# Performance work log

Hardware: AMD Instinct MI355X
Metric: run time of the kernel (lower is better)

Reference implementation:

```python
import jax, jax.numpy as jnp
import numpy as np

DIM = 1024
HEADS = 16
DIM_HEAD = 64
INNER = HEADS * DIM_HEAD
B, N = 2, 2048


def setup_inputs() -> dict:
    key = jax.random.key(0)
    ks = jax.random.split(key, 5)
    x = jax.random.normal(ks[0], (B, N, DIM), dtype=jnp.float32)
    ln_gamma = jnp.ones((DIM,), dtype=jnp.float32)
    ln_beta = jnp.zeros((DIM,), dtype=jnp.float32)
    # torch Linear: weight [out, in]; store as [in, out] for x @ W
    W_qkv = jax.random.normal(ks[1], (DIM, 3 * INNER), dtype=jnp.float32) * (DIM ** -0.5)
    W_out = jax.random.normal(ks[2], (INNER, DIM), dtype=jnp.float32) * (INNER ** -0.5)
    b_out = jax.random.normal(ks[3], (DIM,), dtype=jnp.float32) * 0.01
    return {"x": x, "ln_gamma": ln_gamma, "ln_beta": ln_beta,
            "W_qkv": W_qkv, "W_out": W_out, "b_out": b_out}


def reference(x, ln_gamma, ln_beta, W_qkv, W_out, b_out):
    eps = 1e-5
    scale = DIM_HEAD ** -0.5
    # LayerNorm over last dim
    mu = jnp.mean(x, axis=-1, keepdims=True)
    var = jnp.mean((x - mu) ** 2, axis=-1, keepdims=True)
    xn = (x - mu) * jax.lax.rsqrt(var + eps) * ln_gamma + ln_beta
    # QKV projection (no bias), split
    qkv = xn @ W_qkv                               # [B, N, 3*inner]
    q, k, v = jnp.split(qkv, 3, axis=-1)           # each [B, N, inner]
    def heads(t):
        return t.reshape(B, N, HEADS, DIM_HEAD).transpose(0, 2, 1, 3)  # [B, H, N, d]
    q, k, v = heads(q), heads(k), heads(v)
    dots = jnp.einsum("bhnd,bhmd->bhnm", q, k) * scale
    a = jax.nn.softmax(dots, axis=-1)
    out = jnp.einsum("bhnm,bhmd->bhnd", a, v)      # [B, H, N, d]
    out = out.transpose(0, 2, 1, 3).reshape(B, N, INNER)
    return out @ W_out + b_out                     # dropout p=0 -> identity
```

## Files before the change

kernel.cpp:

```cpp
#include <hip/hip_runtime.h>

typedef unsigned short U16;
typedef __bf16 bf16x8 __attribute__((ext_vector_type(8)));
typedef float f32x4 __attribute__((ext_vector_type(4)));

__device__ inline float b2f(U16 u) {
    union { unsigned int i; float f; } v;
    v.i = ((unsigned int)u) << 16;
    return v.f;
}
__device__ inline U16 f2b(float f) {
    union { float f; unsigned int u; } v;
    v.f = f;
    unsigned int r = (v.u + 0x7fffu + ((v.u >> 16) & 1u)) >> 16;
    return (U16)r;
}

__device__ inline void gld16(const void* g, void* l) {
    __builtin_amdgcn_global_load_lds(
        (const __attribute__((address_space(1))) void*)g,
        (__attribute__((address_space(3))) void*)l, 16, 0, 0);
}

__global__ void transpose_f2b(const float* __restrict__ in, U16* __restrict__ out,
                              int R, int C) {
    __shared__ float tile[32][33];
    int c0 = blockIdx.x * 32, r0 = blockIdx.y * 32;
    int tx = threadIdx.x, ty = threadIdx.y;
#pragma unroll
    for (int i = 0; i < 32; i += 8)
        tile[ty + i][tx] = in[(size_t)(r0 + ty + i) * C + c0 + tx];
    __syncthreads();
#pragma unroll
    for (int i = 0; i < 32; i += 8)
        out[(size_t)(c0 + ty + i) * R + r0 + tx] = f2b(tile[tx][ty + i]);
}

__global__ __launch_bounds__(256) void ln_kernel(const float* __restrict__ x,
                                                 const float* __restrict__ gamma,
                                                 const float* __restrict__ beta,
                                                 U16* __restrict__ xn) {
    int row = blockIdx.x;
    int t = threadIdx.x;
    float4 raw = ((const float4*)(x + (size_t)row * 1024))[t];
    float v[4] = { raw.x, raw.y, raw.z, raw.w };
    float s = v[0] + v[1] + v[2] + v[3];
    float s2 = v[0] * v[0] + v[1] * v[1] + v[2] * v[2] + v[3] * v[3];
#pragma unroll
    for (int off = 32; off >= 1; off >>= 1) {
        s  += __shfl_xor(s,  off);
        s2 += __shfl_xor(s2, off);
    }
    __shared__ float red[8];
    if ((t & 63) == 0) { red[(t >> 6) * 2] = s; red[(t >> 6) * 2 + 1] = s2; }
    __syncthreads();
    float S  = red[0] + red[2] + red[4] + red[6];
    float S2 = red[1] + red[3] + red[5] + red[7];
    float mu = S * (1.0f / 1024.0f);
    float var = S2 * (1.0f / 1024.0f) - mu * mu;
    float rstd = rsqrtf(var + 1e-5f);
    float4 g4 = ((const float4*)gamma)[t];
    float4 b4 = ((const float4*)beta)[t];
    ushort4 o;
    o.x = f2b((v[0] - mu) * rstd * g4.x + b4.x);
    o.y = f2b((v[1] - mu) * rstd * g4.y + b4.y);
    o.z = f2b((v[2] - mu) * rstd * g4.z + b4.z);
    o.w = f2b((v[3] - mu) * rstd * g4.w + b4.w);
    ((ushort4*)(xn + (size_t)row * 1024))[t] = o;
}

template <typename OutT>
__global__ __launch_bounds__(256) void gemm_bt(const U16* __restrict__ A,
                                               const U16* __restrict__ Bt,
                                               const float* __restrict__ bias,
                                               OutT* __restrict__ C,
                                               U16* __restrict__ vT,
                                               int M, int N, int K) {
    __shared__ __align__(16) U16 As[128 * 32];
    __shared__ __align__(16) U16 Bs[128 * 32];
    const int m0 = blockIdx.y * 128, n0 = blockIdx.x * 128;
    const int t = threadIdx.x;
    const int wave = t >> 6, lane = t & 63, l15 = lane & 15, quad = lane >> 4;
    const int wm = (wave >> 1) * 64, wn = (wave & 1) * 64;

    f32x4 acc[4][4];
#pragma unroll
    for (int i = 0; i < 4; i++)
#pragma unroll
        for (int j = 0; j < 4; j++)
            acc[i][j] = (f32x4){0.f, 0.f, 0.f, 0.f};

    const int c0i = t, c1i = 256 + t;
    const int r0 = c0i >> 2, kq0 = c0i & 3;
    const int r1 = c1i >> 2, kq1 = c1i & 3;

    for (int k0 = 0; k0 < K; k0 += 32) {
        gld16(&A[(size_t)(m0 + r0) * K + k0 + kq0 * 8], &As[c0i * 8]);
        gld16(&Bt[(size_t)(n0 + r0) * K + k0 + kq0 * 8], &Bs[c0i * 8]);
        gld16(&A[(size_t)(m0 + r1) * K + k0 + kq1 * 8], &As[c1i * 8]);
        gld16(&Bt[(size_t)(n0 + r1) * K + k0 + kq1 * 8], &Bs[c1i * 8]);
        __syncthreads();
        bf16x8 af[4], bfr[4];
#pragma unroll
        for (int i = 0; i < 4; i++)
            af[i] = *(const bf16x8*)&As[(wm + i * 16 + l15) * 32 + quad * 8];
#pragma unroll
        for (int j = 0; j < 4; j++)
            bfr[j] = *(const bf16x8*)&Bs[(wn + j * 16 + l15) * 32 + quad * 8];
#pragma unroll
        for (int i = 0; i < 4; i++)
#pragma unroll
            for (int j = 0; j < 4; j++)
                acc[i][j] = __builtin_amdgcn_mfma_f32_16x16x32_bf16(
                    af[i], bfr[j], acc[i][j], 0, 0, 0);
        __syncthreads();
    }
    if (vT && n0 >= 2048) {
#pragma unroll
        for (int i = 0; i < 4; i++) {
#pragma unroll
            for (int j = 0; j < 4; j++) {
                int col = n0 + wn + j * 16 + l15 - 2048;
                int hh = col >> 6, dd = col & 63;
                int row0 = m0 + wm + i * 16 + quad * 4;
                int bb = row0 >> 11, nn = row0 & 2047;
                ushort4 st;
                st.x = f2b(acc[i][j][0]); st.y = f2b(acc[i][j][1]);
                st.z = f2b(acc[i][j][2]); st.w = f2b(acc[i][j][3]);
                *(ushort4*)&vT[((((size_t)bb * 16) + hh) * 64 + dd) * 2048 + nn] = st;
            }
        }
        return;
    }
#pragma unroll
    for (int i = 0; i < 4; i++) {
#pragma unroll
        for (int j = 0; j < 4; j++) {
            int col = n0 + wn + j * 16 + l15;
            float bv = bias ? bias[col] : 0.0f;
#pragma unroll
            for (int r = 0; r < 4; r++) {
                int row = m0 + wm + i * 16 + quad * 4 + r;
                float val = acc[i][j][r] + bv;
                if constexpr (sizeof(OutT) == 4)
                    C[(size_t)row * N + col] = val;
                else
                    C[(size_t)row * N + col] = f2b(val);
            }
        }
    }
}

#define PSTR 72
__global__ __launch_bounds__(256) void attn_kernel(const U16* __restrict__ qkv,
                                                   const U16* __restrict__ vT,
                                                   U16* __restrict__ attn_out) {
    const int qt = blockIdx.x;
    const int bh = blockIdx.y;
    const int b = bh >> 4, h = bh & 15;
    const int t = threadIdx.x;
    const int wave = t >> 6, lane = t & 63, l15 = lane & 15, quad = lane >> 4;
    const float sc2 = 0.125f * 1.44269504089f;

    __shared__ __align__(16) U16 Kt[2][64 * 64];
    __shared__ __align__(16) U16 Vt[2][64 * 64];
    __shared__ __align__(16) U16 Pb[4][32 * PSTR];

    const size_t base = (size_t)(b * 2048) * 3072;
    const U16* vTbh = vT + ((size_t)(b * 16 + h) * 64) * 2048;

    bf16x8 qf[2][2];
#pragma unroll
    for (int rf = 0; rf < 2; rf++) {
        int qrow = qt * 128 + wave * 32 + rf * 16 + l15;
        const U16* qp = qkv + base + (size_t)qrow * 3072 + h * 64;
        qf[rf][0] = *(const bf16x8*)&qp[quad * 8];
        qf[rf][1] = *(const bf16x8*)&qp[32 + quad * 8];
    }

    float l_i[2][4];
    f32x4 o[2][4];
#pragma unroll
    for (int rf = 0; rf < 2; rf++) {
#pragma unroll
        for (int r = 0; r < 4; r++) l_i[rf][r] = 0.0f;
#pragma unroll
        for (int f = 0; f < 4; f++) o[rf][f] = (f32x4){0.f, 0.f, 0.f, 0.f};
    }

    const int c0 = t, c1 = 256 + t;
    const int row0 = c0 >> 3, oct0 = (c0 & 7) ^ (row0 & 7);
    const int row1 = c1 >> 3, oct1 = (c1 & 7) ^ (row1 & 7);
    const int s0 = (quad ^ (l15 & 7)) * 8;

    gld16(&qkv[base + (size_t)row0 * 3072 + 1024 + h * 64 + oct0 * 8], &Kt[0][c0 * 8]);
    gld16(&qkv[base + (size_t)row1 * 3072 + 1024 + h * 64 + oct1 * 8], &Kt[0][c1 * 8]);
    gld16(&vTbh[(size_t)row0 * 2048 + oct0 * 8], &Vt[0][c0 * 8]);
    gld16(&vTbh[(size_t)row1 * 2048 + oct1 * 8], &Vt[0][c1 * 8]);
    __syncthreads();

    for (int kt = 0; kt < 32; kt++) {
        {
            int nt = (kt + 1) & 31, nb = (kt + 1) & 1;
            gld16(&qkv[base + (size_t)(nt * 64 + row0) * 3072 + 1024 + h * 64 + oct0 * 8], &Kt[nb][c0 * 8]);
            gld16(&qkv[base + (size_t)(nt * 64 + row1) * 3072 + 1024 + h * 64 + oct1 * 8], &Kt[nb][c1 * 8]);
            gld16(&vTbh[(size_t)row0 * 2048 + nt * 64 + oct0 * 8], &Vt[nb][c0 * 8]);
            gld16(&vTbh[(size_t)row1 * 2048 + nt * 64 + oct1 * 8], &Vt[nb][c1 * 8]);
        }
        const U16* KtC = &Kt[kt & 1][0];
        const U16* VtC = &Vt[kt & 1][0];

        bf16x8 k0[4], k1[4];
#pragma unroll
        for (int c = 0; c < 4; c++) {
            k0[c] = *(const bf16x8*)&KtC[(c * 16 + l15) * 64 + s0];
            k1[c] = *(const bf16x8*)&KtC[(c * 16 + l15) * 64 + (s0 ^ 32)];
        }
        U16* pb = &Pb[wave][0];
#pragma unroll
        for (int rf = 0; rf < 2; rf++) {
            f32x4 s[4];
#pragma unroll
            for (int c = 0; c < 4; c++) {
                f32x4 z = (f32x4){0.f, 0.f, 0.f, 0.f};
                z = __builtin_amdgcn_mfma_f32_16x16x32_bf16(qf[rf][0], k0[c], z, 0, 0, 0);
                z = __builtin_amdgcn_mfma_f32_16x16x32_bf16(qf[rf][1], k1[c], z, 0, 0, 0);
                s[c] = z;
            }
#pragma unroll
            for (int r = 0; r < 4; r++) {
#pragma unroll
                for (int c = 0; c < 4; c++) {
                    float p = __builtin_amdgcn_exp2f(s[c][r] * sc2);
                    l_i[rf][r] += p;
                    union { float f; unsigned int u; } cv; cv.f = p;
                    pb[(rf * 16 + quad * 4 + r) * PSTR + c * 16 + l15] = (U16)(cv.u >> 16);
                }
            }
        }

        asm volatile("s_waitcnt lgkmcnt(0)" ::: "memory");

        bf16x8 vf0[4], vf1[4];
#pragma unroll
        for (int f = 0; f < 4; f++) {
            vf0[f] = *(const bf16x8*)&VtC[(f * 16 + l15) * 64 + s0];
            vf1[f] = *(const bf16x8*)&VtC[(f * 16 + l15) * 64 + (s0 ^ 32)];
        }
#pragma unroll
        for (int rf = 0; rf < 2; rf++) {
            bf16x8 pf0 = *(const bf16x8*)&pb[(rf * 16 + l15) * PSTR + quad * 8];
            bf16x8 pf1 = *(const bf16x8*)&pb[(rf * 16 + l15) * PSTR + 32 + quad * 8];
#pragma unroll
            for (int f = 0; f < 4; f++) {
                o[rf][f] = __builtin_amdgcn_mfma_f32_16x16x32_bf16(pf0, vf0[f], o[rf][f], 0, 0, 0);
                o[rf][f] = __builtin_amdgcn_mfma_f32_16x16x32_bf16(pf1, vf1[f], o[rf][f], 0, 0, 0);
            }
        }
        __syncthreads();
    }

#pragma unroll
    for (int rf = 0; rf < 2; rf++) {
#pragma unroll
        for (int r = 0; r < 4; r++) {
            float l = l_i[rf][r];
#pragma unroll
            for (int off = 8; off >= 1; off >>= 1)
                l += __shfl_xor(l, off, 16);
            l_i[rf][r] = 1.0f / l;
        }
#pragma unroll
        for (int f = 0; f < 4; f++) {
#pragma unroll
            for (int r = 0; r < 4; r++) {
                int row = b * 2048 + qt * 128 + wave * 32 + rf * 16 + quad * 4 + r;
                int col = h * 64 + f * 16 + l15;
                attn_out[(size_t)row * 1024 + col] = f2b(o[rf][f][r] * l_i[rf][r]);
            }
        }
    }
}

extern "C" void kernel_launch(void* const* d_in, const int* in_sizes, int n_in,
                              void* d_out, int out_size, void* d_ws, size_t ws_size,
                              hipStream_t stream) {
    (void)in_sizes; (void)n_in; (void)out_size; (void)ws_size;
    const float* x    = (const float*)d_in[0];
    const float* g    = (const float*)d_in[1];
    const float* be   = (const float*)d_in[2];
    const float* Wqkv = (const float*)d_in[3];
    const float* Wout = (const float*)d_in[4];
    const float* bout = (const float*)d_in[5];
    float* out = (float*)d_out;
    char* ws = (char*)d_ws;

    U16* xn   = (U16*)(ws);
    U16* qkv  = (U16*)(ws + (size_t)(8u  << 20));
    U16* WqT  = (U16*)(ws + (size_t)(32u << 20));
    U16* WoT  = (U16*)(ws + (size_t)(38u << 20));
    U16* vT   = (U16*)(ws + (size_t)(40u << 20));
    U16* aout = xn;

    transpose_f2b<<<dim3(3072 / 32, 1024 / 32), dim3(32, 8), 0, stream>>>(Wqkv, WqT, 1024, 3072);
    transpose_f2b<<<dim3(1024 / 32, 1024 / 32), dim3(32, 8), 0, stream>>>(Wout, WoT, 1024, 1024);
    ln_kernel<<<4096, 256, 0, stream>>>(x, g, be, xn);
    gemm_bt<U16><<<dim3(3072 / 128, 4096 / 128), 256, 0, stream>>>(xn, WqT, nullptr, qkv, vT, 4096, 3072, 1024);
    attn_kernel<<<dim3(16, 32), 256, 0, stream>>>(qkv, vT, aout);
    gemm_bt<float><<<dim3(1024 / 128, 4096 / 128), 256, 0, stream>>>(aout, WoT, bout, out, nullptr, 4096, 1024, 1024);
}
```

Before: 217.3 us.

## Split attention over KV halves with merge kernel, XCD-aware block mapping and setprio

Splits each attention block's 32 KV tiles into two halves processed by separate blocks, doubling the grid to 1024 blocks. Each half writes unnormalized fp32 partial outputs and row sums, and a new merge kernel adds them, normalizes, and writes bf16. This is valid without max-subtraction because the softmax uses no running max, so the partials combine by simple addition. It also remaps block IDs so the heads are grouped per XCD for L2 locality, hoists the V fragment loads earlier, and wraps the MFMA sections in s_setprio. The cost is extra fp32 global traffic, since partials go through the output buffer and workspace, plus one more kernel launch.

```diff
diff --git a/kernel.cpp b/kernel.cpp
--- a/kernel.cpp
+++ b/kernel.cpp
@@ -154,9 +154,16 @@
 #define PSTR 72
 __global__ __launch_bounds__(256) void attn_kernel(const U16* __restrict__ qkv,
                                                    const U16* __restrict__ vT,
-                                                   U16* __restrict__ attn_out) {
-    const int qt = blockIdx.x;
-    const int bh = blockIdx.y;
+                                                   float* __restrict__ po0,
+                                                   float* __restrict__ po1,
+                                                   float* __restrict__ pl) {
+    const int p = blockIdx.x;
+    const int xcd = p & 7;
+    const int slot = p >> 3;
+    const int bh = ((slot & 3) << 3) | xcd;
+    const int r2 = slot >> 2;
+    const int qt = r2 & 15;
+    const int half = r2 >> 4;
     const int b = bh >> 4, h = bh & 15;
     const int t = threadIdx.x;
     const int wave = t >> 6, lane = t & 63, l15 = lane & 15, quad = lane >> 4;
@@ -168,6 +175,7 @@
 
     const size_t base = (size_t)(b * 2048) * 3072;
     const U16* vTbh = vT + ((size_t)(b * 16 + h) * 64) * 2048;
+    const int kbase = half * 16;
 
     bf16x8 qf[2][2];
 #pragma unroll
@@ -193,22 +201,25 @@
     const int row1 = c1 >> 3, oct1 = (c1 & 7) ^ (row1 & 7);
     const int s0 = (quad ^ (l15 & 7)) * 8;
 
-    gld16(&qkv[base + (size_t)row0 * 3072 + 1024 + h * 64 + oct0 * 8], &Kt[0][c0 * 8]);
-    gld16(&qkv[base + (size_t)row1 * 3072 + 1024 + h * 64 + oct1 * 8], &Kt[0][c1 * 8]);
-    gld16(&vTbh[(size_t)row0 * 2048 + oct0 * 8], &Vt[0][c0 * 8]);
-    gld16(&vTbh[(size_t)row1 * 2048 + oct1 * 8], &Vt[0][c1 * 8]);
+    {
+        int nt = kbase;
+        gld16(&qkv[base + (size_t)(nt * 64 + row0) * 3072 + 1024 + h * 64 + oct0 * 8], &Kt[0][c0 * 8]);
+        gld16(&qkv[base + (size_t)(nt * 64 + row1) * 3072 + 1024 + h * 64 + oct1 * 8], &Kt[0][c1 * 8]);
+        gld16(&vTbh[(size_t)row0 * 2048 + nt * 64 + oct0 * 8], &Vt[0][c0 * 8]);
+        gld16(&vTbh[(size_t)row1 * 2048 + nt * 64 + oct1 * 8], &Vt[0][c1 * 8]);
+    }
     __syncthreads();
 
-    for (int kt = 0; kt < 32; kt++) {
+    for (int i = 0; i < 16; i++) {
         {
-            int nt = (kt + 1) & 31, nb = (kt + 1) & 1;
+            int nt = kbase + ((i + 1) & 15), nb = (i + 1) & 1;
             gld16(&qkv[base + (size_t)(nt * 64 + row0) * 3072 + 1024 + h * 64 + oct0 * 8], &Kt[nb][c0 * 8]);
             gld16(&qkv[base + (size_t)(nt * 64 + row1) * 3072 + 1024 + h * 64 + oct1 * 8], &Kt[nb][c1 * 8]);
             gld16(&vTbh[(size_t)row0 * 2048 + nt * 64 + oct0 * 8], &Vt[nb][c0 * 8]);
             gld16(&vTbh[(size_t)row1 * 2048 + nt * 64 + oct1 * 8], &Vt[nb][c1 * 8]);
         }
-        const U16* KtC = &Kt[kt & 1][0];
-        const U16* VtC = &Vt[kt & 1][0];
+        const U16* KtC = &Kt[i & 1][0];
+        const U16* VtC = &Vt[i & 1][0];
 
         bf16x8 k0[4], k1[4];
 #pragma unroll
@@ -216,24 +227,37 @@
             k0[c] = *(const bf16x8*)&KtC[(c * 16 + l15) * 64 + s0];
             k1[c] = *(const bf16x8*)&KtC[(c * 16 + l15) * 64 + (s0 ^ 32)];
         }
-        U16* pb = &Pb[wave][0];
+        bf16x8 vf0[4], vf1[4];
+#pragma unroll
+        for (int f = 0; f < 4; f++) {
+            vf0[f] = *(const bf16x8*)&VtC[(f * 16 + l15) * 64 + s0];
+            vf1[f] = *(const bf16x8*)&VtC[(f * 16 + l15) * 64 + (s0 ^ 32)];
+        }
+
+        f32x4 s[2][4];
+        __builtin_amdgcn_s_setprio(1);
 #pragma unroll
         for (int rf = 0; rf < 2; rf++) {
-            f32x4 s[4];
 #pragma unroll
             for (int c = 0; c < 4; c++) {
                 f32x4 z = (f32x4){0.f, 0.f, 0.f, 0.f};
                 z = __builtin_amdgcn_mfma_f32_16x16x32_bf16(qf[rf][0], k0[c], z, 0, 0, 0);
                 z = __builtin_amdgcn_mfma_f32_16x16x32_bf16(qf[rf][1], k1[c], z, 0, 0, 0);
-                s[c] = z;
-            }
+                s[rf][c] = z;
+            }
+        }
+        __builtin_amdgcn_s_setprio(0);
+
+        U16* pb = &Pb[wave][0];
+#pragma unroll
+        for (int rf = 0; rf < 2; rf++) {
 #pragma unroll
             for (int r = 0; r < 4; r++) {
 #pragma unroll
                 for (int c = 0; c < 4; c++) {
-                    float p = __builtin_amdgcn_exp2f(s[c][r] * sc2);
-                    l_i[rf][r] += p;
-                    union { float f; unsigned int u; } cv; cv.f = p;
+                    float pe = __builtin_amdgcn_exp2f(s[rf][c][r] * sc2);
+                    l_i[rf][r] += pe;
+                    union { float f; unsigned int u; } cv; cv.f = pe;
                     pb[(rf * 16 + quad * 4 + r) * PSTR + c * 16 + l15] = (U16)(cv.u >> 16);
                 }
             }
@@ -241,12 +265,7 @@
 
         asm volatile("s_waitcnt lgkmcnt(0)" ::: "memory");
 
-        bf16x8 vf0[4], vf1[4];
-#pragma unroll
-        for (int f = 0; f < 4; f++) {
-            vf0[f] = *(const bf16x8*)&VtC[(f * 16 + l15) * 64 + s0];
-            vf1[f] = *(const bf16x8*)&VtC[(f * 16 + l15) * 64 + (s0 ^ 32)];
-        }
+        __builtin_amdgcn_s_setprio(1);
 #pragma unroll
         for (int rf = 0; rf < 2; rf++) {
             bf16x8 pf0 = *(const bf16x8*)&pb[(rf * 16 + l15) * PSTR + quad * 8];
@@ -257,6 +276,7 @@
                 o[rf][f] = __builtin_amdgcn_mfma_f32_16x16x32_bf16(pf1, vf1[f], o[rf][f], 0, 0, 0);
             }
         }
+        __builtin_amdgcn_s_setprio(0);
         __syncthreads();
     }
 
@@ -268,18 +288,47 @@
 #pragma unroll
             for (int off = 8; off >= 1; off >>= 1)
                 l += __shfl_xor(l, off, 16);
-            l_i[rf][r] = 1.0f / l;
-        }
+            l_i[rf][r] = l;
+        }
+    }
+    float* po_h = half ? po1 : po0;
+#pragma unroll
+    for (int rf = 0; rf < 2; rf++) {
 #pragma unroll
         for (int f = 0; f < 4; f++) {
 #pragma unroll
             for (int r = 0; r < 4; r++) {
                 int row = b * 2048 + qt * 128 + wave * 32 + rf * 16 + quad * 4 + r;
                 int col = h * 64 + f * 16 + l15;
-                attn_out[(size_t)row * 1024 + col] = f2b(o[rf][f][r] * l_i[rf][r]);
-            }
-        }
-    }
+                po_h[(size_t)row * 1024 + col] = o[rf][f][r];
+            }
+        }
+        if (l15 == 0) {
+#pragma unroll
+            for (int r = 0; r < 4; r++) {
+                int row = b * 2048 + qt * 128 + wave * 32 + rf * 16 + quad * 4 + r;
+                pl[((size_t)half * 4096 + row) * 16 + h] = l_i[rf][r];
+            }
+        }
+    }
+}
+
+__global__ __launch_bounds__(256) void merge_kernel(const float* __restrict__ po0,
+                                                    const float* __restrict__ po1,
+                                                    const float* __restrict__ pl,
+                                                    U16* __restrict__ aout) {
+    int row = blockIdx.x;
+    int t = threadIdx.x;
+    int h = t >> 4;
+    float inv = 1.0f / (pl[(size_t)row * 16 + h] + pl[((size_t)4096 + row) * 16 + h]);
+    float4 a = ((const float4*)(po0 + (size_t)row * 1024))[t];
+    float4 c = ((const float4*)(po1 + (size_t)row * 1024))[t];
+    ushort4 o;
+    o.x = f2b((a.x + c.x) * inv);
+    o.y = f2b((a.y + c.y) * inv);
+    o.z = f2b((a.z + c.z) * inv);
+    o.w = f2b((a.w + c.w) * inv);
+    ((ushort4*)(aout + (size_t)row * 1024))[t] = o;
 }
 
 extern "C" void kernel_launch(void* const* d_in, const int* in_sizes, int n_in,
@@ -300,12 +349,16 @@
     U16* WqT  = (U16*)(ws + (size_t)(32u << 20));
     U16* WoT  = (U16*)(ws + (size_t)(38u << 20));
     U16* vT   = (U16*)(ws + (size_t)(40u << 20));
+    float* po1 = (float*)(ws + (size_t)(48u << 20));
+    float* pl  = (float*)(ws + (size_t)(64u << 20));
     U16* aout = xn;
+    float* po0 = out;
 
     transpose_f2b<<<dim3(3072 / 32, 1024 / 32), dim3(32, 8), 0, stream>>>(Wqkv, WqT, 1024, 3072);
     transpose_f2b<<<dim3(1024 / 32, 1024 / 32), dim3(32, 8), 0, stream>>>(Wout, WoT, 1024, 1024);
     ln_kernel<<<4096, 256, 0, stream>>>(x, g, be, xn);
     gemm_bt<U16><<<dim3(3072 / 128, 4096 / 128), 256, 0, stream>>>(xn, WqT, nullptr, qkv, vT, 4096, 3072, 1024);
-    attn_kernel<<<dim3(16, 32), 256, 0, stream>>>(qkv, vT, aout);
+    attn_kernel<<<dim3(1024), 256, 0, stream>>>(qkv, vT, po0, po1, pl);
+    merge_kernel<<<dim3(4096), 256, 0, stream>>>(po0, po1, pl, aout);
     gemm_bt<float><<<dim3(1024 / 128, 4096 / 128), 256, 0, stream>>>(aout, WoT, bout, out, nullptr, 4096, 1024, 1024);
 }
```

New measurement: 226.6 us. 1.04x slower.
